# Performance work log

Measured on AMD Instinct MI355X. Metric: run time of the kernel, lower is better.

## Reference

```python
import jax, jax.numpy as jnp
import numpy as np

B, TK, H = 32, 1024, 512
N = 2 * H          # hidden_dim * 2
AD = 512           # attention_dimension


def setup_inputs() -> dict:
    key = jax.random.key(0)
    ks = jax.random.split(key, 11)
    s = 0.02  # weight scale
    return {
        's_t_hat': jax.random.normal(ks[0], (B, N), jnp.float32),
        'encoder_outputs': jax.random.normal(ks[1], (B, TK, N), jnp.float32),
        'encoder_feature': jax.random.normal(ks[2], (B * TK, N), jnp.float32),
        'enc_padding_mask': jax.random.uniform(ks[3], (B, TK), jnp.float32),
        'coverage': jax.random.uniform(ks[4], (B, TK), jnp.float32),
        'r_i': jax.random.normal(ks[5], (B, TK, AD), jnp.float32),
        'W_s_w': jax.random.normal(ks[6], (N, N), jnp.float32) * s,
        'W_s_b': jax.random.normal(ks[7], (N,), jnp.float32) * s,
        'W_c_w': jax.random.normal(ks[8], (N, 1), jnp.float32) * s,
        'v_w': jax.random.normal(ks[9], (1, N), jnp.float32) * s,
        'W_r_w': jax.random.normal(ks[10], (N, AD), jnp.float32) * s,
    }


def reference(s_t_hat, encoder_outputs, encoder_feature, enc_padding_mask,
              coverage, r_i, W_s_w, W_s_b, W_c_w, v_w, W_r_w):
    b, t_k, n = encoder_outputs.shape
    # decoder feature: W_s(s_t_hat), broadcast over time
    dec_fea = s_t_hat @ W_s_w.T + W_s_b                       # [b, n]
    enc_feat = encoder_feature.reshape(b, t_k, n)             # [b, t_k, n]
    # coverage feature: W_c applied to scalar coverage per position
    cov_feat = coverage[..., None] * W_c_w[:, 0]              # [b, t_k, n]
    e = jnp.tanh(enc_feat + dec_fea[:, None, :] + cov_feat)   # [b, t_k, n]
    scores = jnp.einsum('btn,n->bt', e, v_w[0])               # [b, t_k]
    attn_ = jax.nn.softmax(scores, axis=1) * enc_padding_mask
    attn = attn_ / attn_.sum(1, keepdims=True)                # renormalized
    c_t = jnp.einsum('bt,btn->bn', attn, encoder_outputs)     # [b, n]
    coverage_new = coverage + attn                            # [b, t_k]
    # structural (LSA) branch
    Wrri = jnp.einsum('bta,na->btn', r_i, W_r_w)              # [b, t_k, n]
    e_s = jnp.tanh(Wrri + dec_fea[:, None, :])
    s2 = jnp.einsum('btn,n->bt', e_s, v_w[0])
    a_struct = (jax.nn.softmax(s2, axis=1) * enc_padding_mask)[:, None, :]  # [b,1,t_k]
    c_t_struct = jnp.einsum('bt,btn->bn', a_struct[:, 0], encoder_outputs)  # [b, n]
    return (c_t, attn, coverage_new, c_t_struct, a_struct)
```

## Files before the change

kernel.cpp:

```cpp
#include <hip/hip_runtime.h>
#include <hip/hip_bf16.h>

static constexpr int BB   = 32;
static constexpr int TKK  = 1024;
static constexpr int ND   = 1024;
static constexpr int ADIM = 512;

typedef __attribute__((ext_vector_type(8))) short bf16x8;
typedef __attribute__((ext_vector_type(4))) float f32x4;

__device__ __forceinline__ float fast_tanh(float x) {
  x = fminf(fmaxf(x, -15.f), 15.f);
  float e = __expf(2.f * x);
  return __fdividef(e - 1.f, e + 1.f);
}

__device__ __forceinline__ short f2bf(float x) {
  unsigned u = __float_as_uint(x);
  u += 0x7FFF + ((u >> 16) & 1);
  return (short)(u >> 16);
}

__device__ __forceinline__ void gload_lds16(const void* g, void* l) {
  __builtin_amdgcn_global_load_lds(
      (const __attribute__((address_space(1))) unsigned int*)g,
      (__attribute__((address_space(3))) unsigned int*)l, 16, 0, 0);
}

__global__ __launch_bounds__(256) void k_cvt(const float* __restrict__ src,
    short* __restrict__ dst) {
  size_t i = (size_t)blockIdx.x * 256 + threadIdx.x;
  float4 a = ((const float4*)src)[2 * i];
  float4 b = ((const float4*)src)[2 * i + 1];
  bf16x8 h;
  h[0] = f2bf(a.x); h[1] = f2bf(a.y); h[2] = f2bf(a.z); h[3] = f2bf(a.w);
  h[4] = f2bf(b.x); h[5] = f2bf(b.y); h[6] = f2bf(b.z); h[7] = f2bf(b.w);
  ((bf16x8*)dst)[i] = h;
}

__global__ __launch_bounds__(256) void k_decfea(const float* __restrict__ s_t_hat,
    const float* __restrict__ Wsw, const float* __restrict__ Wsb,
    float* __restrict__ dec) {
  int b  = blockIdx.x >> 3;
  int n0 = (blockIdx.x & 7) << 7;
  int w = threadIdx.x >> 6, lane = threadIdx.x & 63;
  const float4* s4 = (const float4*)(s_t_hat + (size_t)b * ND);
  float4 sv0 = s4[lane], sv1 = s4[lane + 64], sv2 = s4[lane + 128], sv3 = s4[lane + 192];
  for (int nn = 0; nn < 32; nn++) {
    int n = n0 + w * 32 + nn;
    const float4* w4 = (const float4*)(Wsw + (size_t)n * ND);
    float4 wa = w4[lane], wb = w4[lane + 64], wc = w4[lane + 128], wd = w4[lane + 192];
    float acc = sv0.x*wa.x + sv0.y*wa.y + sv0.z*wa.z + sv0.w*wa.w
              + sv1.x*wb.x + sv1.y*wb.y + sv1.z*wb.z + sv1.w*wb.w
              + sv2.x*wc.x + sv2.y*wc.y + sv2.z*wc.z + sv2.w*wc.w
              + sv3.x*wd.x + sv3.y*wd.y + sv3.z*wd.z + sv3.w*wd.w;
    #pragma unroll
    for (int off = 32; off; off >>= 1) acc += __shfl_down(acc, off);
    if (lane == 0) dec[b * ND + n] = acc + Wsb[n];
  }
}

__global__ __launch_bounds__(256) void k_scoresA(const float* __restrict__ ef,
    const float* __restrict__ dec, const float* __restrict__ Wc,
    const float* __restrict__ vw, const float* __restrict__ cov,
    float* __restrict__ scores) {
  __shared__ float sb[4];
  int bt = blockIdx.x;
  int b  = bt >> 10;
  int tid = threadIdx.x;
  float4 e = *(const float4*)(ef + (size_t)bt * ND + tid * 4);
  float4 d = *(const float4*)(dec + (size_t)b * ND + tid * 4);
  float4 w = *(const float4*)(Wc + tid * 4);
  float4 v = *(const float4*)(vw + tid * 4);
  float c = cov[bt];
  float s = v.x * fast_tanh(e.x + d.x + c * w.x)
          + v.y * fast_tanh(e.y + d.y + c * w.y)
          + v.z * fast_tanh(e.z + d.z + c * w.z)
          + v.w * fast_tanh(e.w + d.w + c * w.w);
  #pragma unroll
  for (int off = 32; off; off >>= 1) s += __shfl_down(s, off);
  if ((tid & 63) == 0) sb[tid >> 6] = s;
  __syncthreads();
  if (tid == 0) scores[bt] = sb[0] + sb[1] + sb[2] + sb[3];
}

__global__ __launch_bounds__(256) void k_softmaxA(const float* __restrict__ scores,
    const float* __restrict__ mask, const float* __restrict__ cov,
    float* __restrict__ attn, float* __restrict__ covnew) {
  __shared__ float sb[4];
  int b = blockIdx.x, tid = threadIdx.x;
  float4 s = *(const float4*)(scores + (size_t)b * TKK + tid * 4);
  float m = fmaxf(fmaxf(s.x, s.y), fmaxf(s.z, s.w));
  #pragma unroll
  for (int off = 32; off; off >>= 1) m = fmaxf(m, __shfl_down(m, off));
  if ((tid & 63) == 0) sb[tid >> 6] = m;
  __syncthreads();
  m = fmaxf(fmaxf(sb[0], sb[1]), fmaxf(sb[2], sb[3]));
  float4 mk = *(const float4*)(mask + (size_t)b * TKK + tid * 4);
  float4 e;
  e.x = __expf(s.x - m) * mk.x;
  e.y = __expf(s.y - m) * mk.y;
  e.z = __expf(s.z - m) * mk.z;
  e.w = __expf(s.w - m) * mk.w;
  float sum = e.x + e.y + e.z + e.w;
  #pragma unroll
  for (int off = 32; off; off >>= 1) sum += __shfl_down(sum, off);
  __syncthreads();
  if ((tid & 63) == 0) sb[tid >> 6] = sum;
  __syncthreads();
  float inv = __fdividef(1.f, sb[0] + sb[1] + sb[2] + sb[3]);
  float4 a = {e.x * inv, e.y * inv, e.z * inv, e.w * inv};
  *(float4*)(attn + (size_t)b * TKK + tid * 4) = a;
  float4 c = *(const float4*)(cov + (size_t)b * TKK + tid * 4);
  float4 cn = {c.x + a.x, c.y + a.y, c.z + a.z, c.w + a.w};
  *(float4*)(covnew + (size_t)b * TKK + tid * 4) = cn;
}

__global__ __launch_bounds__(256) void k_gemmB3(const short* __restrict__ rb,
    const short* __restrict__ wb, const float* __restrict__ dec,
    const float* __restrict__ vw, float* __restrict__ part) {
  __shared__ __align__(16) short As[2][128 * 64];
  __shared__ __align__(16) short Bs[2][128 * 64];
  const int tid = threadIdx.x;
  const int lane = tid & 63, wv = tid >> 6;
  const int wm = wv >> 1, wn = wv & 1;
  const int g = lane >> 4, cl = lane & 15;
  const int mchunk = blockIdx.x, nchunk = blockIdx.y;
  const int b  = mchunk >> 3;
  const int t0 = (mchunk & 7) * 128;
  const int n0 = nchunk * 128;
  const int srow8  = lane >> 3;
  const int sk     = ((lane & 7) ^ srow8) * 8;
  const short* Agbase = rb + (size_t)(b * TKK + t0) * ADIM;
  const short* Bgbase = wb + (size_t)n0 * ADIM;
  const int rsw = (cl & 7) << 3;

  f32x4 acc[4][4];
  #pragma unroll
  for (int m = 0; m < 4; ++m)
    #pragma unroll
    for (int n = 0; n < 4; ++n) acc[m][n] = (f32x4){0.f, 0.f, 0.f, 0.f};

  auto stage = [&](int buf, int kc) {
    const int k0 = kc * 64;
    #pragma unroll
    for (int p = 0; p < 4; ++p) {
      const int rowc = p * 32 + wv * 8;
      const int row  = rowc + srow8;
      gload_lds16(Agbase + (size_t)row * ADIM + k0 + sk, &As[buf][rowc * 64]);
      gload_lds16(Bgbase + (size_t)row * ADIM + k0 + sk, &Bs[buf][rowc * 64]);
    }
  };

  stage(0, 0);
  for (int kc = 0; kc < 8; ++kc) {
    const int cur = kc & 1;
    if (kc < 7) {
      stage(cur ^ 1, kc + 1);
      asm volatile("s_waitcnt vmcnt(8)" ::: "memory");
    } else {
      asm volatile("s_waitcnt vmcnt(0)" ::: "memory");
    }
    __builtin_amdgcn_s_barrier();
    #pragma unroll
    for (int kf = 0; kf < 2; ++kf) {
      bf16x8 af[4], bfr[4];
      #pragma unroll
      for (int m = 0; m < 4; ++m)
        af[m] = *(const bf16x8*)&As[cur][(wm * 64 + m * 16 + cl) * 64
                                         + (((kf * 4 + g) * 8) ^ rsw)];
      #pragma unroll
      for (int n = 0; n < 4; ++n)
        bfr[n] = *(const bf16x8*)&Bs[cur][(wn * 64 + n * 16 + cl) * 64
                                          + (((kf * 4 + g) * 8) ^ rsw)];
      #pragma unroll
      for (int m = 0; m < 4; ++m)
        #pragma unroll
        for (int n = 0; n < 4; ++n)
          acc[m][n] = __builtin_amdgcn_mfma_f32_16x16x32_bf16(af[m], bfr[n], acc[m][n], 0, 0, 0);
    }
    __builtin_amdgcn_s_barrier();
  }

  float vvv[4], ddd[4];
  #pragma unroll
  for (int n = 0; n < 4; ++n) {
    const int col = n0 + wn * 64 + n * 16 + cl;
    vvv[n] = vw[col];
    ddd[n] = dec[b * ND + col];
  }
  #pragma unroll
  for (int m = 0; m < 4; ++m) {
    #pragma unroll
    for (int r = 0; r < 4; ++r) {
      float s = 0.f;
      #pragma unroll
      for (int n = 0; n < 4; ++n)
        s += vvv[n] * fast_tanh(acc[m][n][r] + ddd[n]);
      #pragma unroll
      for (int off = 1; off < 16; off <<= 1) s += __shfl_xor(s, off);
      if (cl == 0) {
        const int rowg = b * TKK + t0 + wm * 64 + m * 16 + g * 4 + r;
        part[(size_t)rowg * 16 + nchunk * 2 + wn] = s;
      }
    }
  }
}

__global__ __launch_bounds__(256) void k_gemmB(const float* __restrict__ r_i,
    const float* __restrict__ Wr, const float* __restrict__ dec,
    const float* __restrict__ vw, float* __restrict__ part) {
  __shared__ short As[128 * 64];
  __shared__ short Bs[128 * 64];
  const int tid = threadIdx.x;
  const int lane = tid & 63, wv = tid >> 6;
  const int wm = wv >> 1, wn = wv & 1;
  const int g = lane >> 4, cl = lane & 15;
  const int mchunk = blockIdx.x, nchunk = blockIdx.y;
  const int b  = mchunk >> 3;
  const int t0 = (mchunk & 7) * 128;
  const int n0 = nchunk * 128;
  const float* Ag = r_i + (size_t)(b * TKK + t0) * ADIM;
  const float* Bg = Wr + (size_t)n0 * ADIM;
  const int srow = tid >> 3, skk = (tid & 7) * 8;

  f32x4 acc[4][4];
  #pragma unroll
  for (int m = 0; m < 4; ++m)
    #pragma unroll
    for (int n = 0; n < 4; ++n) acc[m][n] = (f32x4){0.f, 0.f, 0.f, 0.f};

  for (int kc = 0; kc < 8; ++kc) {
    const int k0 = kc * 64;
    __syncthreads();
    #pragma unroll
    for (int dit = 0; dit < 4; ++dit) {
      const int row = dit * 32 + srow;
      const float* sa = Ag + (size_t)row * ADIM + k0 + skk;
      float4 a0 = *(const float4*)sa, a1 = *(const float4*)(sa + 4);
      bf16x8 ha;
      ha[0]=f2bf(a0.x); ha[1]=f2bf(a0.y); ha[2]=f2bf(a0.z); ha[3]=f2bf(a0.w);
      ha[4]=f2bf(a1.x); ha[5]=f2bf(a1.y); ha[6]=f2bf(a1.z); ha[7]=f2bf(a1.w);
      *(bf16x8*)&As[row * 64 + skk] = ha;
      const float* sbp = Bg + (size_t)row * ADIM + k0 + skk;
      float4 b0 = *(const float4*)sbp, b1 = *(const float4*)(sbp + 4);
      bf16x8 hb;
      hb[0]=f2bf(b0.x); hb[1]=f2bf(b0.y); hb[2]=f2bf(b0.z); hb[3]=f2bf(b0.w);
      hb[4]=f2bf(b1.x); hb[5]=f2bf(b1.y); hb[6]=f2bf(b1.z); hb[7]=f2bf(b1.w);
      *(bf16x8*)&Bs[row * 64 + skk] = hb;
    }
    __syncthreads();
    #pragma unroll
    for (int kf = 0; kf < 2; ++kf) {
      bf16x8 af[4], bfr[4];
      #pragma unroll
      for (int m = 0; m < 4; ++m)
        af[m] = *(const bf16x8*)&As[(wm * 64 + m * 16 + cl) * 64 + kf * 32 + g * 8];
      #pragma unroll
      for (int n = 0; n < 4; ++n)
        bfr[n] = *(const bf16x8*)&Bs[(wn * 64 + n * 16 + cl) * 64 + kf * 32 + g * 8];
      #pragma unroll
      for (int m = 0; m < 4; ++m)
        #pragma unroll
        for (int n = 0; n < 4; ++n)
          acc[m][n] = __builtin_amdgcn_mfma_f32_16x16x32_bf16(af[m], bfr[n], acc[m][n], 0, 0, 0);
    }
  }
  float vvv[4], ddd[4];
  #pragma unroll
  for (int n = 0; n < 4; ++n) {
    const int col = n0 + wn * 64 + n * 16 + cl;
    vvv[n] = vw[col];
    ddd[n] = dec[b * ND + col];
  }
  #pragma unroll
  for (int m = 0; m < 4; ++m) {
    #pragma unroll
    for (int r = 0; r < 4; ++r) {
      float s = 0.f;
      #pragma unroll
      for (int n = 0; n < 4; ++n)
        s += vvv[n] * fast_tanh(acc[m][n][r] + ddd[n]);
      #pragma unroll
      for (int off = 1; off < 16; off <<= 1) s += __shfl_xor(s, off);
      if (cl == 0) {
        const int rowg = b * TKK + t0 + wm * 64 + m * 16 + g * 4 + r;
        part[(size_t)rowg * 16 + nchunk * 2 + wn] = s;
      }
    }
  }
}

__global__ __launch_bounds__(256) void k_softmaxB(const float* __restrict__ part,
    const float* __restrict__ mask, float* __restrict__ astruct) {
  __shared__ float sb[4];
  int b = blockIdx.x, tid = threadIdx.x;
  float sv[4];
  #pragma unroll
  for (int tt = 0; tt < 4; ++tt) {
    const float4* pp = (const float4*)(part + ((size_t)b * TKK + tid * 4 + tt) * 16);
    float4 q0 = pp[0], q1 = pp[1], q2 = pp[2], q3 = pp[3];
    sv[tt] = q0.x+q0.y+q0.z+q0.w + q1.x+q1.y+q1.z+q1.w
           + q2.x+q2.y+q2.z+q2.w + q3.x+q3.y+q3.z+q3.w;
  }
  float m = fmaxf(fmaxf(sv[0], sv[1]), fmaxf(sv[2], sv[3]));
  #pragma unroll
  for (int off = 32; off; off >>= 1) m = fmaxf(m, __shfl_down(m, off));
  if ((tid & 63) == 0) sb[tid >> 6] = m;
  __syncthreads();
  m = fmaxf(fmaxf(sb[0], sb[1]), fmaxf(sb[2], sb[3]));
  float e0 = __expf(sv[0] - m), e1 = __expf(sv[1] - m);
  float e2 = __expf(sv[2] - m), e3 = __expf(sv[3] - m);
  float sum = e0 + e1 + e2 + e3;
  #pragma unroll
  for (int off = 32; off; off >>= 1) sum += __shfl_down(sum, off);
  __syncthreads();
  if ((tid & 63) == 0) sb[tid >> 6] = sum;
  __syncthreads();
  float inv = __fdividef(1.f, sb[0] + sb[1] + sb[2] + sb[3]);
  float4 mk = *(const float4*)(mask + (size_t)b * TKK + tid * 4);
  float4 a = {e0 * mk.x * inv, e1 * mk.y * inv, e2 * mk.z * inv, e3 * mk.w * inv};
  *(float4*)(astruct + (size_t)b * TKK + tid * 4) = a;
}

__global__ __launch_bounds__(256) void k_ctx(const float* __restrict__ enc,
    const float* __restrict__ attn, const float* __restrict__ astr,
    float* __restrict__ partials) {
  int tc = blockIdx.x, b = blockIdx.y;
  int tid = threadIdx.x, lane = tid & 63;
  float a1v = attn[(size_t)b * TKK + tc * 64 + lane];
  float a2v = astr[(size_t)b * TKK + tc * 64 + lane];
  const float4* e4 = (const float4*)(enc + (size_t)(b * TKK + tc * 64) * ND);
  float4 ac = {0, 0, 0, 0}, as = {0, 0, 0, 0};
  #pragma unroll 4
  for (int m = 0; m < 64; m++) {
    float a1 = __shfl(a1v, m), a2 = __shfl(a2v, m);
    float4 ev = e4[(size_t)m * 256 + tid];
    ac.x += a1 * ev.x; ac.y += a1 * ev.y; ac.z += a1 * ev.z; ac.w += a1 * ev.w;
    as.x += a2 * ev.x; as.y += a2 * ev.y; as.z += a2 * ev.z; as.w += a2 * ev.w;
  }
  float* p = partials + (size_t)(b * 16 + tc) * 2 * ND;
  *(float4*)(p + tid * 4) = ac;
  *(float4*)(p + ND + tid * 4) = as;
}

__global__ __launch_bounds__(256) void k_reduce(const float* __restrict__ partials,
    float* __restrict__ ct, float* __restrict__ cts) {
  int b = blockIdx.x, tid = threadIdx.x;
  float4 sc = {0, 0, 0, 0}, ss = {0, 0, 0, 0};
  for (int tc = 0; tc < 16; tc++) {
    const float* p = partials + (size_t)(b * 16 + tc) * 2 * ND;
    float4 p1 = *(const float4*)(p + tid * 4);
    float4 p2 = *(const float4*)(p + ND + tid * 4);
    sc.x += p1.x; sc.y += p1.y; sc.z += p1.z; sc.w += p1.w;
    ss.x += p2.x; ss.y += p2.y; ss.z += p2.z; ss.w += p2.w;
  }
  *(float4*)(ct + (size_t)b * ND + tid * 4) = sc;
  *(float4*)(cts + (size_t)b * ND + tid * 4) = ss;
}

extern "C" void kernel_launch(void* const* d_in, const int* in_sizes, int n_in,
                              void* d_out, int out_size, void* d_ws, size_t ws_size,
                              hipStream_t stream) {
  const float* s_t_hat = (const float*)d_in[0];
  const float* enc_out  = (const float*)d_in[1];
  const float* enc_feat = (const float*)d_in[2];
  const float* mask     = (const float*)d_in[3];
  const float* cov      = (const float*)d_in[4];
  const float* r_i      = (const float*)d_in[5];
  const float* Wsw      = (const float*)d_in[6];
  const float* Wsb      = (const float*)d_in[7];
  const float* Wc       = (const float*)d_in[8];
  const float* vw       = (const float*)d_in[9];
  const float* Wr       = (const float*)d_in[10];

  float* out    = (float*)d_out;
  float* ct     = out;
  float* attn   = out + 32768;
  float* covnew = out + 65536;
  float* cts    = out + 98304;
  float* astr   = out + 131072;

  float* ws       = (float*)d_ws;
  float* dec      = ws;
  float* scores   = ws + 32768;
  float* s2part   = ws + 65536;
  float* partials = ws + 589824;
  short* rb       = (short*)(ws + 1638400);
  short* wb       = rb + 16777216;
  const size_t NEEDED = 1638400ull * 4 + 16777216ull * 2 + 524288ull * 2;

  k_decfea<<<256, 256, 0, stream>>>(s_t_hat, Wsw, Wsb, dec);
  k_scoresA<<<BB * TKK, 256, 0, stream>>>(enc_feat, dec, Wc, vw, cov, scores);
  k_softmaxA<<<BB, 256, 0, stream>>>(scores, mask, cov, attn, covnew);
  if (ws_size >= NEEDED) {
    k_cvt<<<8192, 256, 0, stream>>>(r_i, rb);
    k_cvt<<<256, 256, 0, stream>>>(Wr, wb);
    k_gemmB3<<<dim3(256, 8), 256, 0, stream>>>(rb, wb, dec, vw, s2part);
  } else {
    k_gemmB<<<dim3(256, 8), 256, 0, stream>>>(r_i, Wr, dec, vw, s2part);
  }
  k_softmaxB<<<BB, 256, 0, stream>>>(s2part, mask, astr);
  k_ctx<<<dim3(16, BB), 256, 0, stream>>>(enc_out, attn, astr, partials);
  k_reduce<<<BB, 256, 0, stream>>>(partials, ct, cts);
}
```

Baseline: 181.8 us.

## Halve GEMM K-tile to 32 and merge the two bf16 convert launches

The bf16 GEMM for the structural branch now stages 32-wide K slices instead of 64. That halves the LDS footprint per block, which may allow more resident blocks, and it gets a matching new XOR swizzle for both the global-to-LDS loads and the fragment reads. In exchange the loop runs twice as many iterations, so there are twice as many barriers and waits per block. The two separate float-to-bf16 conversion launches for r_i and W_r are also fused into one kernel that branches on block index, removing one launch.

```diff
diff --git a/kernel.cpp b/kernel.cpp
--- a/kernel.cpp
+++ b/kernel.cpp
@@ -27,9 +27,14 @@
       (__attribute__((address_space(3))) unsigned int*)l, 16, 0, 0);
 }
 
-__global__ __launch_bounds__(256) void k_cvt(const float* __restrict__ src,
-    short* __restrict__ dst) {
-  size_t i = (size_t)blockIdx.x * 256 + threadIdx.x;
+__global__ __launch_bounds__(256) void k_cvt2(const float* __restrict__ r_i,
+    const float* __restrict__ Wr, short* __restrict__ rb, short* __restrict__ wb) {
+  size_t bid = blockIdx.x;
+  const float* src;
+  short* dst;
+  size_t i;
+  if (bid < 8192) { src = r_i; dst = rb; i = bid * 256 + threadIdx.x; }
+  else            { src = Wr;  dst = wb; i = (bid - 8192) * 256 + threadIdx.x; }
   float4 a = ((const float4*)src)[2 * i];
   float4 b = ((const float4*)src)[2 * i + 1];
   bf16x8 h;
@@ -119,8 +124,8 @@
 __global__ __launch_bounds__(256) void k_gemmB3(const short* __restrict__ rb,
     const short* __restrict__ wb, const float* __restrict__ dec,
     const float* __restrict__ vw, float* __restrict__ part) {
-  __shared__ __align__(16) short As[2][128 * 64];
-  __shared__ __align__(16) short Bs[2][128 * 64];
+  __shared__ __align__(16) short As[2][128 * 32];
+  __shared__ __align__(16) short Bs[2][128 * 32];
   const int tid = threadIdx.x;
   const int lane = tid & 63, wv = tid >> 6;
   const int wm = wv >> 1, wn = wv & 1;
@@ -129,11 +134,11 @@
   const int b  = mchunk >> 3;
   const int t0 = (mchunk & 7) * 128;
   const int n0 = nchunk * 128;
-  const int srow8  = lane >> 3;
-  const int sk     = ((lane & 7) ^ srow8) * 8;
+  const int lrow4 = lane >> 2;
+  const int sck   = ((lane & 3) ^ ((lane >> 3) & 3)) * 8;
   const short* Agbase = rb + (size_t)(b * TKK + t0) * ADIM;
   const short* Bgbase = wb + (size_t)n0 * ADIM;
-  const int rsw = (cl & 7) << 3;
+  const int rdsw = (g ^ ((cl >> 1) & 3)) * 8;
 
   f32x4 acc[4][4];
   #pragma unroll
@@ -142,43 +147,38 @@
     for (int n = 0; n < 4; ++n) acc[m][n] = (f32x4){0.f, 0.f, 0.f, 0.f};
 
   auto stage = [&](int buf, int kc) {
-    const int k0 = kc * 64;
-    #pragma unroll
-    for (int p = 0; p < 4; ++p) {
-      const int rowc = p * 32 + wv * 8;
-      const int row  = rowc + srow8;
-      gload_lds16(Agbase + (size_t)row * ADIM + k0 + sk, &As[buf][rowc * 64]);
-      gload_lds16(Bgbase + (size_t)row * ADIM + k0 + sk, &Bs[buf][rowc * 64]);
+    const int k0 = kc * 32;
+    #pragma unroll
+    for (int p = 0; p < 2; ++p) {
+      const int rowc = p * 64 + wv * 16;
+      const int row  = rowc + lrow4;
+      gload_lds16(Agbase + (size_t)row * ADIM + k0 + sck, &As[buf][rowc * 32]);
+      gload_lds16(Bgbase + (size_t)row * ADIM + k0 + sck, &Bs[buf][rowc * 32]);
     }
   };
 
   stage(0, 0);
-  for (int kc = 0; kc < 8; ++kc) {
+  for (int kc = 0; kc < 16; ++kc) {
     const int cur = kc & 1;
-    if (kc < 7) {
+    if (kc < 15) {
       stage(cur ^ 1, kc + 1);
-      asm volatile("s_waitcnt vmcnt(8)" ::: "memory");
+      asm volatile("s_waitcnt vmcnt(4)" ::: "memory");
     } else {
       asm volatile("s_waitcnt vmcnt(0)" ::: "memory");
     }
     __builtin_amdgcn_s_barrier();
-    #pragma unroll
-    for (int kf = 0; kf < 2; ++kf) {
-      bf16x8 af[4], bfr[4];
-      #pragma unroll
-      for (int m = 0; m < 4; ++m)
-        af[m] = *(const bf16x8*)&As[cur][(wm * 64 + m * 16 + cl) * 64
-                                         + (((kf * 4 + g) * 8) ^ rsw)];
+    bf16x8 af[4], bfr[4];
+    #pragma unroll
+    for (int m = 0; m < 4; ++m)
+      af[m] = *(const bf16x8*)&As[cur][(wm * 64 + m * 16 + cl) * 32 + rdsw];
+    #pragma unroll
+    for (int n = 0; n < 4; ++n)
+      bfr[n] = *(const bf16x8*)&Bs[cur][(wn * 64 + n * 16 + cl) * 32 + rdsw];
+    #pragma unroll
+    for (int m = 0; m < 4; ++m)
       #pragma unroll
       for (int n = 0; n < 4; ++n)
-        bfr[n] = *(const bf16x8*)&Bs[cur][(wn * 64 + n * 16 + cl) * 64
-                                          + (((kf * 4 + g) * 8) ^ rsw)];
-      #pragma unroll
-      for (int m = 0; m < 4; ++m)
-        #pragma unroll
-        for (int n = 0; n < 4; ++n)
-          acc[m][n] = __builtin_amdgcn_mfma_f32_16x16x32_bf16(af[m], bfr[n], acc[m][n], 0, 0, 0);
-    }
+        acc[m][n] = __builtin_amdgcn_mfma_f32_16x16x32_bf16(af[m], bfr[n], acc[m][n], 0, 0, 0);
     __builtin_amdgcn_s_barrier();
   }
 
@@ -394,8 +394,7 @@
   k_scoresA<<<BB * TKK, 256, 0, stream>>>(enc_feat, dec, Wc, vw, cov, scores);
   k_softmaxA<<<BB, 256, 0, stream>>>(scores, mask, cov, attn, covnew);
   if (ws_size >= NEEDED) {
-    k_cvt<<<8192, 256, 0, stream>>>(r_i, rb);
-    k_cvt<<<256, 256, 0, stream>>>(Wr, wb);
+    k_cvt2<<<8448, 256, 0, stream>>>(r_i, Wr, rb, wb);
     k_gemmB3<<<dim3(256, 8), 256, 0, stream>>>(rb, wb, dec, vw, s2part);
   } else {
     k_gemmB<<<dim3(256, 8), 256, 0, stream>>>(r_i, Wr, dec, vw, s2part);
```

Result: faster. 176.3 us (-3.0%).
